# Optimization experiments

Hardware: AMD Instinct MI355X
Metric: run time of the kernel (lower is better)

## Reference

```python
import jax, jax.numpy as jnp
import numpy as np

NEG_BIG = -9e15
LRELU_SLOPE = 0.2  # alpha

N = 8192
IN_F = 256
OUT_F = 128


def setup_inputs() -> dict:
    key = jax.random.key(0)
    k1, k2, k3, k4 = jax.random.split(key, 4)
    inputs = jax.random.normal(k1, (N, IN_F), dtype=jnp.float32)
    adj = jax.random.randint(k2, (N, N), 0, 2, dtype=jnp.int32)
    # xavier_uniform with gain=1.414
    gain = 1.414
    bW = gain * np.sqrt(6.0 / (IN_F + OUT_F))
    W = jax.random.uniform(k3, (IN_F, OUT_F), minval=-bW, maxval=bW, dtype=jnp.float32)
    ba = gain * np.sqrt(6.0 / (2 * OUT_F + 1))
    a = jax.random.uniform(k4, (2 * OUT_F, 1), minval=-ba, maxval=ba, dtype=jnp.float32)
    return {"inputs": inputs, "adj": adj, "W": W, "a": a}


def reference(inputs, adj, W, a):
    # h: [N, F']
    h = inputs @ W
    # a^T [h_i || h_j] = h_i . a[:F'] + h_j . a[F':]  -- avoids the O(N^2 * 2F') concat
    a1 = a[:OUT_F, 0]   # [F']
    a2 = a[OUT_F:, 0]   # [F']
    s1 = h @ a1         # [N]
    s2 = h @ a2         # [N]
    e = s1[:, None] + s2[None, :]                      # [N, N]
    e = jnp.where(e >= 0, e, LRELU_SLOPE * e)          # LeakyReLU(alpha)
    scores = jnp.where(adj > 0, e, jnp.float32(NEG_BIG))
    attention = jax.nn.softmax(scores, axis=1)         # row softmax; dropout p=0
    h_prime = attention @ h                            # [N, F']
    return jax.nn.elu(h_prime)                         # concat=True -> elu
```

## Files before the change

### kernel.cpp

```cpp
#include <hip/hip_runtime.h>
#include <hip/hip_bf16.h>

#define NN   8192
#define INF_ 256
#define OUTF 128
#define SLOPE 0.2f
#define NJC  4
#define JCHUNK (NN / NJC)
#define NT   (JCHUNK / 128)

typedef float f32x4  __attribute__((ext_vector_type(4)));
typedef float f32x16 __attribute__((ext_vector_type(16)));
typedef short bf16x8 __attribute__((ext_vector_type(8)));
typedef int   i32x4  __attribute__((ext_vector_type(4)));
typedef unsigned int u32;
typedef unsigned short u16;
typedef u16 u16x4 __attribute__((ext_vector_type(4)));

__device__ __forceinline__ u16 f2bf(float f) {
  return __builtin_bit_cast(u16, __float2bfloat16(f));
}


__global__ __launch_bounds__(256) void gat_k1(
    const float* __restrict__ X, const float* __restrict__ W,
    const float* __restrict__ a, u16* __restrict__ hbF,
    float* __restrict__ s1, float* __restrict__ s2) {
  __shared__ float xs[32 * INF_];
  const int t = threadIdx.x;
  const int r0 = blockIdx.x * 32;
  {
    const f32x4* src = (const f32x4*)(X + (size_t)r0 * INF_);
    f32x4* dst = (f32x4*)xs;
    for (int i = t; i < 32 * INF_ / 4; i += 256) dst[i] = src[i];
  }
  __syncthreads();
  const int cg = t & 31;
  const int rg = t >> 5;
  float acc[4][4];
#pragma unroll
  for (int i = 0; i < 4; i++)
#pragma unroll
    for (int j = 0; j < 4; j++) acc[i][j] = 0.f;

  for (int k = 0; k < INF_; k += 4) {
    f32x4 xv[4];
#pragma unroll
    for (int i = 0; i < 4; i++) xv[i] = *(const f32x4*)&xs[(rg * 4 + i) * INF_ + k];
#pragma unroll
    for (int kk = 0; kk < 4; kk++) {
      f32x4 wv = *(const f32x4*)&W[(k + kk) * OUTF + cg * 4];
#pragma unroll
      for (int i = 0; i < 4; i++)
#pragma unroll
        for (int j = 0; j < 4; j++) acc[i][j] = fmaf(xv[i][kk], wv[j], acc[i][j]);
    }
  }

  f32x4 a1v = *(const f32x4*)&a[cg * 4];
  f32x4 a2v = *(const f32x4*)&a[OUTF + cg * 4];
  float p1[4], p2[4];
#pragma unroll
  for (int i = 0; i < 4; i++) {
    p1[i] = acc[i][0] * a1v[0] + acc[i][1] * a1v[1] + acc[i][2] * a1v[2] + acc[i][3] * a1v[3];
    p2[i] = acc[i][0] * a2v[0] + acc[i][1] * a2v[1] + acc[i][2] * a2v[2] + acc[i][3] * a2v[3];
  }
#pragma unroll
  for (int m = 1; m < 32; m <<= 1) {
#pragma unroll
    for (int i = 0; i < 4; i++) {
      p1[i] += __shfl_xor(p1[i], m);
      p2[i] += __shfl_xor(p2[i], m);
    }
  }
  if (cg == 0) {
#pragma unroll
    for (int i = 0; i < 4; i++) {
      s1[r0 + rg * 4 + i] = p1[i];
      s2[r0 + rg * 4 + i] = p2[i];
    }
  }

  const int R0 = r0 + rg * 4;
  const int jg = (R0 & 2047) >> 3;
  const int tt = jg & 15;
  const int pr = jg >> 4;
  const int wq = pr >> 1;
  const int gg = pr & 1;
  const int e0 = R0 & 7;
  const int n  = ((R0 >> 11) * 16 + tt) * 8 + wq;
#pragma unroll
  for (int j = 0; j < 4; j++) {
    const int C = cg * 4 + j;
    u16x4 pk;
#pragma unroll
    for (int i = 0; i < 4; i++) pk[i] = f2bf(acc[i][j]);
    size_t flat = ((size_t)(n * 4 + (C >> 5)) * 64 + (C & 31) + 32 * gg) * 8 + e0;
    *(u16x4*)(hbF + flat) = pk;
  }
}

__global__ __launch_bounds__(256) void gat_k2(const float* __restrict__ s2,
                                              float* __restrict__ bmax,
                                              float* __restrict__ E1,
                                              float* __restrict__ E2) {
  __shared__ float sm[4];
  const int t = threadIdx.x;
  const int i = blockIdx.x * 256 + t;
  f32x4 v = ((const f32x4*)s2)[i];
  f32x4 e1, e2;
  float m = -1e30f;
#pragma unroll
  for (int k = 0; k < 4; k++) {
    m = fmaxf(m, v[k]);
    e1[k] = __expf(v[k]);
    e2[k] = __expf(SLOPE * v[k]);
  }
  ((f32x4*)E1)[i] = e1;
  ((f32x4*)E2)[i] = e2;
#pragma unroll
  for (int k = 1; k < 64; k <<= 1) m = fmaxf(m, __shfl_xor(m, k));
  if ((t & 63) == 0) sm[t >> 6] = m;
  __syncthreads();
  if (t == 0)
    bmax[blockIdx.x] = fmaxf(fmaxf(sm[0], sm[1]), fmaxf(sm[2], sm[3]));
}

__device__ __forceinline__ void st16(float* dst, const f32x16& A, int g) {
#pragma unroll
  for (int r = 0; r < 16; r++) {
    const int dr = (r & 3) + 8 * (r >> 2) + 4 * g;
    dst[dr * 128] = A[r];
  }
}
__device__ __forceinline__ void ad16(float* dst, const f32x16& A, int g) {
#pragma unroll
  for (int r = 0; r < 16; r++) {
    const int dr = (r & 3) + 8 * (r >> 2) + 4 * g;
    dst[dr * 128] += A[r];
  }
}

__global__ __launch_bounds__(512, 4) void gat_k3(
    const int* __restrict__ adj, const u16* __restrict__ hbF,
    const float* __restrict__ s1g, const float* __restrict__ E1,
    const float* __restrict__ E2, const float* __restrict__ bmax,
    float* __restrict__ part, float* __restrict__ dpart) {
  __shared__ float lred[8192];
  __shared__ float dred[256];
  const int t = threadIdx.x;
  const int w = t >> 6;
  const int l = t & 63;
  const int rb = blockIdx.x & 255;
  const int jc = blockIdx.x >> 8;
  const int r0 = rb * 32;
  const int row = l & 31;
  const int g = l >> 5;

  unsigned char* bits = (unsigned char*)lred;
  {
    const int prow = t >> 4;
    const int cl = t & 15;
    const int* ap = adj + (size_t)(r0 + prow) * NN + jc * JCHUNK + cl * 8;
#pragma unroll 4
    for (int k = 0; k < 16; k++) {
      i32x4 x0 = *(const i32x4*)(ap + k * 128);
      i32x4 x1 = *(const i32x4*)(ap + k * 128 + 4);
      unsigned b = 0;
#pragma unroll
      for (int e = 0; e < 4; e++) b |= (x0[e] > 0 ? 1u : 0u) << e;
#pragma unroll
      for (int e = 0; e < 4; e++) b |= (x1[e] > 0 ? 1u : 0u) << (e + 4);
      bits[prow * 256 + k * 16 + cl] = (unsigned char)b;
    }
  }
  __syncthreads();

  float s2m = bmax[0];
#pragma unroll
  for (int k = 1; k < 8; k++) s2m = fmaxf(s2m, bmax[k]);
  const float s1r = s1g[r0 + row];
  float Mi = s1r + s2m;
  Mi = fmaxf(Mi, SLOPE * Mi);
  const float A = __expf(s1r - Mi);
  const float B = __expf(SLOPE * s1r - Mi);

  const int pr = 2 * w + g;
  const i32x4 bmv = *(const i32x4*)(bits + row * 256 + pr * 16);
  __syncthreads();

  f32x16 acc0 = 0.f, acc1 = 0.f, acc2 = 0.f, acc3 = 0.f;

  const float* e1p = E1 + jc * JCHUNK + pr * 128;
  const float* e2p = E2 + jc * JCHUNK + pr * 128;
  const bf16x8* bp = (const bf16x8*)hbF + ((size_t)(jc * 128 + w) * 4) * 64 + l;

  float dsA = 0.f, dsB = 0.f;
#pragma unroll
  for (int q4 = 0; q4 < 4; q4++) {
    const unsigned word = (unsigned)bmv[q4];
#pragma unroll
    for (int ti = 0; ti < 4; ti++) {
      const int tt = q4 * 4 + ti;
      const unsigned b = word >> (ti * 8);
      const bf16x8* bq = bp + (size_t)tt * 2048;
      bf16x8 b0 = bq[0], b1 = bq[64], b2 = bq[128], b3 = bq[192];
      f32x4 u0 = *(const f32x4*)(e1p + 8 * tt);
      f32x4 u1 = *(const f32x4*)(e1p + 8 * tt + 4);
      f32x4 v0 = *(const f32x4*)(e2p + 8 * tt);
      f32x4 v1 = *(const f32x4*)(e2p + 8 * tt + 4);
      const float uu[8] = {u0[0], u0[1], u0[2], u0[3], u1[0], u1[1], u1[2], u1[3]};
      const float vv[8] = {v0[0], v0[1], v0[2], v0[3], v1[0], v1[1], v1[2], v1[3]};

      u32 aw[4];
#pragma unroll
      for (int e = 0; e < 8; e += 2) {
        float pa = fmaxf(A * uu[e],     B * vv[e]);
        float pb = fmaxf(A * uu[e + 1], B * vv[e + 1]);
        pa = (b & (1u << e))       ? pa : 0.f;
        pb = (b & (1u << (e + 1))) ? pb : 0.f;
        dsA += pa;
        dsB += pb;
        aw[e >> 1] = __builtin_amdgcn_perm(
            __builtin_bit_cast(u32, pb) + 0x8000u,
            __builtin_bit_cast(u32, pa) + 0x8000u, 0x07060302u);
      }
      const bf16x8 af =
          __builtin_bit_cast(bf16x8, (i32x4){(int)aw[0], (int)aw[1],
                                             (int)aw[2], (int)aw[3]});
      acc0 = __builtin_amdgcn_mfma_f32_32x32x16_bf16(af, b0, acc0, 0, 0, 0);
      acc1 = __builtin_amdgcn_mfma_f32_32x32x16_bf16(af, b1, acc1, 0, 0, 0);
      acc2 = __builtin_amdgcn_mfma_f32_32x32x16_bf16(af, b2, acc2, 0, 0, 0);
      acc3 = __builtin_amdgcn_mfma_f32_32x32x16_bf16(af, b3, acc3, 0, 0, 0);
    }
  }
  float dsum = dsA + dsB;

  dsum += __shfl_xor(dsum, 32);
  if (l < 32) dred[w * 32 + l] = dsum;

  const int colw = l & 31;
  if (w < 2) {
    st16(&lred[w * 4096 + 0 * 32 + colw], acc0, g);
    st16(&lred[w * 4096 + 1 * 32 + colw], acc1, g);
    st16(&lred[w * 4096 + 2 * 32 + colw], acc2, g);
    st16(&lred[w * 4096 + 3 * 32 + colw], acc3, g);
  }
  __syncthreads();
  if (t < 32) {
    float d = 0.f;
#pragma unroll
    for (int w8 = 0; w8 < 8; w8++) d += dred[w8 * 32 + t];
    dpart[jc * NN + r0 + t] = d;
  }
  if (w == 2 || w == 3) {
    ad16(&lred[(w - 2) * 4096 + 0 * 32 + colw], acc0, g);
    ad16(&lred[(w - 2) * 4096 + 1 * 32 + colw], acc1, g);
    ad16(&lred[(w - 2) * 4096 + 2 * 32 + colw], acc2, g);
    ad16(&lred[(w - 2) * 4096 + 3 * 32 + colw], acc3, g);
  }
  __syncthreads();
  if (w == 4 || w == 5) {
    ad16(&lred[(w - 4) * 4096 + 0 * 32 + colw], acc0, g);
    ad16(&lred[(w - 4) * 4096 + 1 * 32 + colw], acc1, g);
    ad16(&lred[(w - 4) * 4096 + 2 * 32 + colw], acc2, g);
    ad16(&lred[(w - 4) * 4096 + 3 * 32 + colw], acc3, g);
  }
  __syncthreads();
  if (w == 6 || w == 7) {
    ad16(&lred[(w - 6) * 4096 + 0 * 32 + colw], acc0, g);
    ad16(&lred[(w - 6) * 4096 + 1 * 32 + colw], acc1, g);
    ad16(&lred[(w - 6) * 4096 + 2 * 32 + colw], acc2, g);
    ad16(&lred[(w - 6) * 4096 + 3 * 32 + colw], acc3, g);
  }
  __syncthreads();

  const int flat = t * 8;
  f32x4 pa = *(f32x4*)&lred[flat];
  f32x4 pb = *(f32x4*)&lred[flat + 4];
  pa += *(f32x4*)&lred[4096 + flat];
  pb += *(f32x4*)&lred[4096 + flat + 4];
  float* pp = part + (size_t)jc * (NN * OUTF) + (size_t)r0 * OUTF + flat;
  *(f32x4*)pp = pa;
  *(f32x4*)(pp + 4) = pb;
}

__global__ __launch_bounds__(256) void gat_k4(
    const float* __restrict__ part, const float* __restrict__ dpart,
    float* __restrict__ out) {
  const int idx = blockIdx.x * 256 + threadIdx.x;
  const int e4 = idx * 4;
  const int i = e4 >> 7;
  f32x4 p = {0.f, 0.f, 0.f, 0.f};
  float d = 0.f;
#pragma unroll
  for (int jc = 0; jc < NJC; jc++) {
    p += *(const f32x4*)&part[(size_t)jc * (NN * OUTF) + e4];
    d += dpart[jc * NN + i];
  }
  d = fmaxf(d, 1e-30f);
  f32x4 r;
#pragma unroll
  for (int k = 0; k < 4; k++) {
    float v = p[k] / d;
    r[k] = (v > 0.f) ? v : expm1f(v);
  }
  *(f32x4*)&out[e4] = r;
}

extern "C" void kernel_launch(void* const* d_in, const int* in_sizes, int n_in,
                              void* d_out, int out_size, void* d_ws, size_t ws_size,
                              hipStream_t stream) {
  (void)in_sizes; (void)n_in; (void)out_size; (void)ws_size;
  const float* X  = (const float*)d_in[0];
  const int*  adj = (const int*)d_in[1];
  const float* W  = (const float*)d_in[2];
  const float* a  = (const float*)d_in[3];
  float* out = (float*)d_out;

  char* ws = (char*)d_ws;
  u16*   hbF   = (u16*)ws;
  float* s1    = (float*)(ws + (2u << 20));
  float* s2    = (float*)(ws + (2u << 20) + (32u << 10));
  float* bmax  = (float*)(ws + (2u << 20) + (64u << 10));
  float* E1    = (float*)(ws + (2u << 20) + (128u << 10));
  float* E2    = (float*)(ws + (2u << 20) + (160u << 10));
  float* dpart = (float*)(ws + (2u << 20) + (192u << 10));
  float* part  = (float*)(ws + (4u << 20));

  gat_k1<<<NN / 32, 256, 0, stream>>>(X, W, a, hbF, s1, s2);
  gat_k2<<<8, 256, 0, stream>>>(s2, bmax, E1, E2);
  gat_k3<<<256 * NJC, 512, 0, stream>>>(adj, hbF, s1, E1, E2, bmax, part, dpart);
  gat_k4<<<(NN * OUTF / 4) / 256, 256, 0, stream>>>(part, dpart, out);
}
```

Baseline: 103.2 us.

## Pipeline adjacency bitmask loads with MFMA loop and split j into eight chunks

The attention kernel now streams the adjacency tile in eight sub-steps, packing the bitmask one step ahead and loading raw adj two steps ahead, so the global reads of the large int32 adjacency matrix overlap with MFMA work instead of finishing before compute starts. The j range is split into eight chunks with 256-thread blocks, giving more blocks and fewer waves per block. The h layout written by the projection kernel is simplified to a linear group layout, and that kernel now processes 16 rows per block. The cost is a barrier per sub-step, twice the partial-sum traffic into the final reduce kernel, and a layout change that both kernels must agree on.

```diff
diff --git a/kernel.cpp b/kernel.cpp
--- a/kernel.cpp
+++ b/kernel.cpp
@@ -5,9 +5,9 @@
 #define INF_ 256
 #define OUTF 128
 #define SLOPE 0.2f
-#define NJC  4
+#define NJC  8
 #define JCHUNK (NN / NJC)
-#define NT   (JCHUNK / 128)
+#define NSUB 8
 
 typedef float f32x4  __attribute__((ext_vector_type(4)));
 typedef float f32x16 __attribute__((ext_vector_type(16)));
@@ -15,7 +15,7 @@
 typedef int   i32x4  __attribute__((ext_vector_type(4)));
 typedef unsigned int u32;
 typedef unsigned short u16;
-typedef u16 u16x4 __attribute__((ext_vector_type(4)));
+typedef u16 u16x2 __attribute__((ext_vector_type(2)));
 
 __device__ __forceinline__ u16 f2bf(float f) {
   return __builtin_bit_cast(u16, __float2bfloat16(f));
@@ -26,32 +26,33 @@
     const float* __restrict__ X, const float* __restrict__ W,
     const float* __restrict__ a, u16* __restrict__ hbF,
     float* __restrict__ s1, float* __restrict__ s2) {
-  __shared__ float xs[32 * INF_];
+  __shared__ float xs[16 * INF_];
   const int t = threadIdx.x;
-  const int r0 = blockIdx.x * 32;
+  const int r0 = blockIdx.x * 16;
   {
     const f32x4* src = (const f32x4*)(X + (size_t)r0 * INF_);
     f32x4* dst = (f32x4*)xs;
-    for (int i = t; i < 32 * INF_ / 4; i += 256) dst[i] = src[i];
+#pragma unroll
+    for (int i = 0; i < 4; i++) dst[t + 256 * i] = src[t + 256 * i];
   }
   __syncthreads();
   const int cg = t & 31;
   const int rg = t >> 5;
-  float acc[4][4];
-#pragma unroll
-  for (int i = 0; i < 4; i++)
+  float acc[2][4];
+#pragma unroll
+  for (int i = 0; i < 2; i++)
 #pragma unroll
     for (int j = 0; j < 4; j++) acc[i][j] = 0.f;
 
   for (int k = 0; k < INF_; k += 4) {
-    f32x4 xv[4];
-#pragma unroll
-    for (int i = 0; i < 4; i++) xv[i] = *(const f32x4*)&xs[(rg * 4 + i) * INF_ + k];
+    f32x4 xv[2];
+#pragma unroll
+    for (int i = 0; i < 2; i++) xv[i] = *(const f32x4*)&xs[(rg * 2 + i) * INF_ + k];
 #pragma unroll
     for (int kk = 0; kk < 4; kk++) {
       f32x4 wv = *(const f32x4*)&W[(k + kk) * OUTF + cg * 4];
 #pragma unroll
-      for (int i = 0; i < 4; i++)
+      for (int i = 0; i < 2; i++)
 #pragma unroll
         for (int j = 0; j < 4; j++) acc[i][j] = fmaf(xv[i][kk], wv[j], acc[i][j]);
     }
@@ -59,44 +60,36 @@
 
   f32x4 a1v = *(const f32x4*)&a[cg * 4];
   f32x4 a2v = *(const f32x4*)&a[OUTF + cg * 4];
-  float p1[4], p2[4];
-#pragma unroll
-  for (int i = 0; i < 4; i++) {
+  float p1[2], p2[2];
+#pragma unroll
+  for (int i = 0; i < 2; i++) {
     p1[i] = acc[i][0] * a1v[0] + acc[i][1] * a1v[1] + acc[i][2] * a1v[2] + acc[i][3] * a1v[3];
     p2[i] = acc[i][0] * a2v[0] + acc[i][1] * a2v[1] + acc[i][2] * a2v[2] + acc[i][3] * a2v[3];
   }
 #pragma unroll
   for (int m = 1; m < 32; m <<= 1) {
 #pragma unroll
-    for (int i = 0; i < 4; i++) {
+    for (int i = 0; i < 2; i++) {
       p1[i] += __shfl_xor(p1[i], m);
       p2[i] += __shfl_xor(p2[i], m);
     }
   }
   if (cg == 0) {
 #pragma unroll
-    for (int i = 0; i < 4; i++) {
-      s1[r0 + rg * 4 + i] = p1[i];
-      s2[r0 + rg * 4 + i] = p2[i];
+    for (int i = 0; i < 2; i++) {
+      s1[r0 + rg * 2 + i] = p1[i];
+      s2[r0 + rg * 2 + i] = p2[i];
     }
   }
 
-  const int R0 = r0 + rg * 4;
-  const int jg = (R0 & 2047) >> 3;
-  const int tt = jg & 15;
-  const int pr = jg >> 4;
-  const int wq = pr >> 1;
-  const int gg = pr & 1;
+  const int R0 = r0 + rg * 2;
+  const int jg = R0 >> 3;
   const int e0 = R0 & 7;
-  const int n  = ((R0 >> 11) * 16 + tt) * 8 + wq;
 #pragma unroll
   for (int j = 0; j < 4; j++) {
     const int C = cg * 4 + j;
-    u16x4 pk;
-#pragma unroll
-    for (int i = 0; i < 4; i++) pk[i] = f2bf(acc[i][j]);
-    size_t flat = ((size_t)(n * 4 + (C >> 5)) * 64 + (C & 31) + 32 * gg) * 8 + e0;
-    *(u16x4*)(hbF + flat) = pk;
+    u16x2 pk = {f2bf(acc[0][j]), f2bf(acc[1][j])};
+    *(u16x2*)(hbF + ((size_t)(jg * 4 + (C >> 5)) * 32 + (C & 31)) * 8 + e0) = pk;
   }
 }
 
@@ -141,13 +134,14 @@
   }
 }
 
-__global__ __launch_bounds__(512, 4) void gat_k3(
+__global__ __launch_bounds__(256, 4) void gat_k3(
     const int* __restrict__ adj, const u16* __restrict__ hbF,
     const float* __restrict__ s1g, const float* __restrict__ E1,
     const float* __restrict__ E2, const float* __restrict__ bmax,
     float* __restrict__ part, float* __restrict__ dpart) {
+  __shared__ unsigned char mbits[4096];
   __shared__ float lred[8192];
-  __shared__ float dred[256];
+  __shared__ float dred[128];
   const int t = threadIdx.x;
   const int w = t >> 6;
   const int l = t & 63;
@@ -156,25 +150,8 @@
   const int r0 = rb * 32;
   const int row = l & 31;
   const int g = l >> 5;
-
-  unsigned char* bits = (unsigned char*)lred;
-  {
-    const int prow = t >> 4;
-    const int cl = t & 15;
-    const int* ap = adj + (size_t)(r0 + prow) * NN + jc * JCHUNK + cl * 8;
-#pragma unroll 4
-    for (int k = 0; k < 16; k++) {
-      i32x4 x0 = *(const i32x4*)(ap + k * 128);
-      i32x4 x1 = *(const i32x4*)(ap + k * 128 + 4);
-      unsigned b = 0;
-#pragma unroll
-      for (int e = 0; e < 4; e++) b |= (x0[e] > 0 ? 1u : 0u) << e;
-#pragma unroll
-      for (int e = 0; e < 4; e++) b |= (x1[e] > 0 ? 1u : 0u) << (e + 4);
-      bits[prow * 256 + k * 16 + cl] = (unsigned char)b;
-    }
-  }
-  __syncthreads();
+  const int x = l & 31;
+  const int pr = 2 * w + g;
 
   float s2m = bmax[0];
 #pragma unroll
@@ -185,30 +162,59 @@
   const float A = __expf(s1r - Mi);
   const float B = __expf(SLOPE * s1r - Mi);
 
-  const int pr = 2 * w + g;
-  const i32x4 bmv = *(const i32x4*)(bits + row * 256 + pr * 16);
-  __syncthreads();
+  const int srow = t >> 3;
+  const int q = t & 7;
+  const int* gsrc = adj + (size_t)(r0 + srow) * NN + jc * JCHUNK + q * 16;
+
+  i32x4 st[4];
+#define LOADS(S)                                   \
+  {                                                \
+    const int* p_ = gsrc + (S) * 128;              \
+    st[0] = *(const i32x4*)(p_);                   \
+    st[1] = *(const i32x4*)(p_ + 4);               \
+    st[2] = *(const i32x4*)(p_ + 8);               \
+    st[3] = *(const i32x4*)(p_ + 12);              \
+  }
+#define PACKW(S)                                                         \
+  {                                                                      \
+    unsigned b0 = 0, b1 = 0;                                             \
+    _Pragma("unroll") for (int e = 0; e < 4; e++) {                      \
+      b0 |= (st[0][e] > 0 ? 1u : 0u) << e;                               \
+      b0 |= (st[1][e] > 0 ? 1u : 0u) << (e + 4);                         \
+      b1 |= (st[2][e] > 0 ? 1u : 0u) << e;                               \
+      b1 |= (st[3][e] > 0 ? 1u : 0u) << (e + 4);                         \
+    }                                                                    \
+    *(u16*)&mbits[(S) * 512 + srow * 16 + q * 2] = (u16)(b0 | (b1 << 8));\
+  }
 
   f32x16 acc0 = 0.f, acc1 = 0.f, acc2 = 0.f, acc3 = 0.f;
-
-  const float* e1p = E1 + jc * JCHUNK + pr * 128;
-  const float* e2p = E2 + jc * JCHUNK + pr * 128;
-  const bf16x8* bp = (const bf16x8*)hbF + ((size_t)(jc * 128 + w) * 4) * 64 + l;
-
   float dsA = 0.f, dsB = 0.f;
-#pragma unroll
-  for (int q4 = 0; q4 < 4; q4++) {
-    const unsigned word = (unsigned)bmv[q4];
-#pragma unroll
-    for (int ti = 0; ti < 4; ti++) {
-      const int tt = q4 * 4 + ti;
-      const unsigned b = word >> (ti * 8);
-      const bf16x8* bq = bp + (size_t)tt * 2048;
-      bf16x8 b0 = bq[0], b1 = bq[64], b2 = bq[128], b3 = bq[192];
-      f32x4 u0 = *(const f32x4*)(e1p + 8 * tt);
-      f32x4 u1 = *(const f32x4*)(e1p + 8 * tt + 4);
-      f32x4 v0 = *(const f32x4*)(e2p + 8 * tt);
-      f32x4 v1 = *(const f32x4*)(e2p + 8 * tt + 4);
+
+  LOADS(0);
+  PACKW(0);
+  LOADS(1);
+  asm volatile("s_waitcnt lgkmcnt(0)" ::: "memory");
+  __builtin_amdgcn_s_barrier();
+
+  for (int s = 0; s < NSUB; s++) {
+    if (s + 1 < NSUB) PACKW(s + 1);
+    if (s + 2 < NSUB) LOADS(s + 2);
+
+#pragma unroll
+    for (int u = 0; u < 2; u++) {
+      const int tt = 2 * s + u;
+      const unsigned b = mbits[s * 512 + row * 16 + u * 8 + pr];
+      const int jg = jc * 128 + tt * 8 + pr;
+      const u16* bqb = hbF + (size_t)jg * 4 * 256 + x * 8;
+      bf16x8 b0 = *(const bf16x8*)(bqb);
+      bf16x8 b1 = *(const bf16x8*)(bqb + 256);
+      bf16x8 b2 = *(const bf16x8*)(bqb + 512);
+      bf16x8 b3 = *(const bf16x8*)(bqb + 768);
+      const int j0 = jc * JCHUNK + tt * 64 + pr * 8;
+      f32x4 u0 = *(const f32x4*)(E1 + j0);
+      f32x4 u1 = *(const f32x4*)(E1 + j0 + 4);
+      f32x4 v0 = *(const f32x4*)(E2 + j0);
+      f32x4 v1 = *(const f32x4*)(E2 + j0 + 4);
       const float uu[8] = {u0[0], u0[1], u0[2], u0[3], u1[0], u1[1], u1[2], u1[3]};
       const float vv[8] = {v0[0], v0[1], v0[2], v0[3], v1[0], v1[1], v1[2], v1[3]};
 
@@ -233,9 +239,12 @@
       acc2 = __builtin_amdgcn_mfma_f32_32x32x16_bf16(af, b2, acc2, 0, 0, 0);
       acc3 = __builtin_amdgcn_mfma_f32_32x32x16_bf16(af, b3, acc3, 0, 0, 0);
     }
-  }
+
+    asm volatile("s_waitcnt lgkmcnt(0)" ::: "memory");
+    __builtin_amdgcn_s_barrier();
+  }
+
   float dsum = dsA + dsB;
-
   dsum += __shfl_xor(dsum, 32);
   if (l < 32) dred[w * 32 + l] = dsum;
 
@@ -250,39 +259,25 @@
   if (t < 32) {
     float d = 0.f;
 #pragma unroll
-    for (int w8 = 0; w8 < 8; w8++) d += dred[w8 * 32 + t];
+    for (int w4 = 0; w4 < 4; w4++) d += dred[w4 * 32 + t];
     dpart[jc * NN + r0 + t] = d;
   }
-  if (w == 2 || w == 3) {
+  if (w >= 2) {
     ad16(&lred[(w - 2) * 4096 + 0 * 32 + colw], acc0, g);
     ad16(&lred[(w - 2) * 4096 + 1 * 32 + colw], acc1, g);
     ad16(&lred[(w - 2) * 4096 + 2 * 32 + colw], acc2, g);
     ad16(&lred[(w - 2) * 4096 + 3 * 32 + colw], acc3, g);
   }
   __syncthreads();
-  if (w == 4 || w == 5) {
-    ad16(&lred[(w - 4) * 4096 + 0 * 32 + colw], acc0, g);
-    ad16(&lred[(w - 4) * 4096 + 1 * 32 + colw], acc1, g);
-    ad16(&lred[(w - 4) * 4096 + 2 * 32 + colw], acc2, g);
-    ad16(&lred[(w - 4) * 4096 + 3 * 32 + colw], acc3, g);
-  }
-  __syncthreads();
-  if (w == 6 || w == 7) {
-    ad16(&lred[(w - 6) * 4096 + 0 * 32 + colw], acc0, g);
-    ad16(&lred[(w - 6) * 4096 + 1 * 32 + colw], acc1, g);
-    ad16(&lred[(w - 6) * 4096 + 2 * 32 + colw], acc2, g);
-    ad16(&lred[(w - 6) * 4096 + 3 * 32 + colw], acc3, g);
-  }
-  __syncthreads();
-
-  const int flat = t * 8;
-  f32x4 pa = *(f32x4*)&lred[flat];
-  f32x4 pb = *(f32x4*)&lred[flat + 4];
-  pa += *(f32x4*)&lred[4096 + flat];
-  pb += *(f32x4*)&lred[4096 + flat + 4];
+
+  const int flat = t * 16;
   float* pp = part + (size_t)jc * (NN * OUTF) + (size_t)r0 * OUTF + flat;
-  *(f32x4*)pp = pa;
-  *(f32x4*)(pp + 4) = pb;
+#pragma unroll
+  for (int i = 0; i < 4; i++) {
+    f32x4 pv = *(f32x4*)&lred[flat + 4 * i];
+    pv += *(f32x4*)&lred[4096 + flat + 4 * i];
+    *(f32x4*)(pp + 4 * i) = pv;
+  }
 }
 
 __global__ __launch_bounds__(256) void gat_k4(
@@ -328,8 +323,8 @@
   float* dpart = (float*)(ws + (2u << 20) + (192u << 10));
   float* part  = (float*)(ws + (4u << 20));
 
-  gat_k1<<<NN / 32, 256, 0, stream>>>(X, W, a, hbF, s1, s2);
+  gat_k1<<<NN / 16, 256, 0, stream>>>(X, W, a, hbF, s1, s2);
   gat_k2<<<8, 256, 0, stream>>>(s2, bmax, E1, E2);
-  gat_k3<<<256 * NJC, 512, 0, stream>>>(adj, hbF, s1, E1, E2, bmax, part, dpart);
+  gat_k3<<<256 * NJC, 256, 0, stream>>>(adj, hbF, s1, E1, E2, bmax, part, dpart);
   gat_k4<<<(NN * OUTF / 4) / 256, 256, 0, stream>>>(part, dpart, out);
 }
```

New measurement: 143.9 us. 1.39x slower.
